# Kernel optimization log

Measured on AMD Instinct MI355X. Metric: run time of the kernel, lower is better.

Reference implementation:

```python
import jax, jax.numpy as jnp
import numpy as np
from jax import lax

TAU = 30.0  # softmax temperature


def setup_inputs() -> dict:
    key = jax.random.key(0)
    ks = jax.random.split(key, 6)
    N, Ci, Co, H, K, KW = 16, 64, 64, 256, 3, 4
    x = jax.random.normal(ks[0], (N, Ci, H, H), jnp.float32)
    # bank of KW candidate kernels: (Co, KW, Ci, K, K), kaiming-ish scale
    w_bank = jax.random.normal(ks[1], (Co, KW, Ci, K, K), jnp.float32) * (2.0 / (Co * K * K)) ** 0.5
    b_bank = jax.random.normal(ks[2], (Co, KW), jnp.float32) * 0.01
    # attention MLP (two 1x1 convs): Ci -> Ci//KW -> KW
    att_w1 = jax.random.normal(ks[3], (Ci // KW, Ci), jnp.float32) * (1.0 / Ci) ** 0.5
    att_b1 = jnp.zeros((Ci // KW,), jnp.float32)
    att_w2 = jax.random.normal(ks[4], (KW, Ci // KW), jnp.float32) * (KW / Ci) ** 0.5
    att_b2 = jnp.zeros((KW,), jnp.float32)
    return {"x": x, "w_bank": w_bank, "b_bank": b_bank,
            "att_w1": att_w1, "att_b1": att_b1, "att_w2": att_w2, "att_b2": att_b2}


def reference(x, w_bank, b_bank, att_w1, att_b1, att_w2, att_b2):
    # attention over weight banks: 1x1 conv -> ReLU -> 1x1 conv -> global avg pool -> softmax(/tau)
    h = jax.nn.relu(jnp.einsum('nchw,dc->ndhw', x, att_w1) + att_b1[None, :, None, None])
    logits = jnp.einsum('ndhw,ed->nehw', h, att_w2) + att_b2[None, :, None, None]
    pooled = jnp.mean(logits, axis=(2, 3))          # [N, KW] (avg_pool2d with kernel=H on square input)
    pi = jax.nn.softmax(pooled / TAU, axis=1)       # [N, KW]
    # per-sample aggregated kernels/biases
    w = jnp.einsum('okcij,nk->nocij', w_bank, pi)   # [N, Co, Ci, K, K]
    b = jnp.einsum('ok,nk->no', b_bank, pi)         # [N, Co]
    # per-sample conv (equivalent to the groups=N conv2d trick)
    def conv_one(xi, wi):
        return lax.conv_general_dilated(xi[None], wi, window_strides=(1, 1),
                                        padding=[(1, 1), (1, 1)],
                                        dimension_numbers=('NCHW', 'OIHW', 'NCHW'))[0]
    y = jax.vmap(conv_one)(x, w)                    # [N, Co, H, W]
    return y + b[:, :, None, None]
```

## Files before the change

kernel.cpp:

```cpp
#include <hip/hip_runtime.h>
#include <hip/hip_bf16.h>

typedef short short8 __attribute__((ext_vector_type(8)));
typedef float f32x4 __attribute__((ext_vector_type(4)));
typedef unsigned short ushort_t;

#define AS1 __attribute__((address_space(1)))
#define AS3 __attribute__((address_space(3)))

__device__ __forceinline__ ushort_t f2bf(float f) {
    unsigned u = __builtin_bit_cast(unsigned, f);
    unsigned r = (u + 0x7FFFu + ((u >> 16) & 1u)) >> 16;
    return (ushort_t)r;
}

__device__ __forceinline__ void gload_lds16(const void* g, void* l) {
    __builtin_amdgcn_global_load_lds((const AS1 unsigned*)g, (AS3 unsigned*)l, 16, 0, 0);
}

__global__ __launch_bounds__(256) void dc_k0_zeroborder(ushort_t* __restrict__ x_t)
{
    const int b = blockIdx.x, t = threadIdx.x;
    const int n = b >> 1, row = (b & 1) ? 257 : 0;
    short8 z = {0, 0, 0, 0, 0, 0, 0, 0};
    short8* p = reinterpret_cast<short8*>(x_t + (size_t)(n * 258 + row) * 258 * 64);
    for (int i = t; i < 2064; i += 256) p[i] = z;
}

__global__ __launch_bounds__(256) void dc_k1_stage_attn(
    const float* __restrict__ x, const float* __restrict__ w1,
    const float* __restrict__ b1, float* __restrict__ s_glob,
    ushort_t* __restrict__ x_t)
{
    __shared__ unsigned xt32[256 * 32];
    __shared__ ushort_t w1s[16 * 64];
    __shared__ float sacc[16];

    const int n = blockIdx.y, h = blockIdx.x, t = threadIdx.x;
    if (t < 16) sacc[t] = 0.f;
#pragma unroll
    for (int q = 0; q < 4; ++q) { int idx = q * 256 + t; w1s[idx] = f2bf(w1[idx]); }

    const float* xr = x + ((size_t)n * 64) * 65536 + (size_t)h * 256;
    const int sw = (t & 7) << 2;
    for (int cp = 0; cp < 32; ++cp) {
        float a = xr[(size_t)(2 * cp) * 65536 + t];
        float b = xr[(size_t)(2 * cp + 1) * 65536 + t];
        xt32[(t * 32 + cp) ^ sw] = (unsigned)f2bf(a) | ((unsigned)f2bf(b) << 16);
    }
    __syncthreads();

    const int lane = t & 63, wv = t >> 6, l15 = lane & 15, lg = lane >> 4;
    const short8* xt8 = reinterpret_cast<const short8*>(xt32);
    const short8* w18 = reinterpret_cast<const short8*>(w1s);

    short8 a0 = w18[l15 * 8 + lg];
    short8 a1 = w18[l15 * 8 + 4 + lg];
    float b1v[4];
#pragma unroll
    for (int r = 0; r < 4; ++r) b1v[r] = b1[lg * 4 + r];

    float rs[4] = {0.f, 0.f, 0.f, 0.f};
#pragma unroll
    for (int q = 0; q < 4; ++q) {
        int px = (wv * 4 + q) * 16 + l15;
        int pb = px * 8, ps = px & 7;
        short8 bb0 = xt8[pb + (lg ^ ps)];
        short8 bb1 = xt8[pb + ((4 + lg) ^ ps)];
        f32x4 hacc = {0.f, 0.f, 0.f, 0.f};
        hacc = __builtin_amdgcn_mfma_f32_16x16x32_bf16(a0, bb0, hacc, 0, 0, 0);
        hacc = __builtin_amdgcn_mfma_f32_16x16x32_bf16(a1, bb1, hacc, 0, 0, 0);
#pragma unroll
        for (int r = 0; r < 4; ++r) rs[r] += fmaxf(hacc[r] + b1v[r], 0.f);
    }
#pragma unroll
    for (int off = 1; off < 16; off <<= 1)
#pragma unroll
        for (int r = 0; r < 4; ++r) rs[r] += __shfl_xor(rs[r], off);
    if (l15 == 0) {
#pragma unroll
        for (int r = 0; r < 4; ++r) atomicAdd(&sacc[lg * 4 + r], rs[r]);
    }
    __syncthreads();
    if (t < 16) atomicAdd(&s_glob[n * 16 + t], sacc[t]);

    ushort_t* xo = x_t + (((size_t)n * 258 + h + 1) * 258 + 1) * 64;
    const int cb = t & 7, pxr = t >> 3;
#pragma unroll
    for (int rr = 0; rr < 8; ++rr) {
        int px = rr * 32 + pxr;
        short8 v = xt8[px * 8 + (cb ^ (px & 7))];
        *reinterpret_cast<short8*>(xo + (size_t)px * 64 + cb * 8) = v;
    }
    if (t < 16) {
        short8 z = {0, 0, 0, 0, 0, 0, 0, 0};
        size_t colbase = (((size_t)n * 258 + h + 1) * 258 + ((t < 8) ? 0 : 257)) * 64;
        reinterpret_cast<short8*>(x_t + colbase)[t & 7] = z;
    }
}

__global__ void dc_k2a_softmax_bias(
    const float* __restrict__ s_glob, const float* __restrict__ w2,
    const float* __restrict__ b2, const float* __restrict__ b_bank,
    float* __restrict__ pi, float* __restrict__ b_agg)
{
    __shared__ float piL[16][4];
    const int t = threadIdx.x;
    if (t < 16) {
        int n = t;
        float z[4];
#pragma unroll
        for (int e = 0; e < 4; ++e) {
            float p = 0.f;
            for (int d = 0; d < 16; ++d) p += w2[e * 16 + d] * s_glob[n * 16 + d];
            z[e] = (b2[e] + p * (1.f / 65536.f)) * (1.f / 30.f);
        }
        float m = fmaxf(fmaxf(z[0], z[1]), fmaxf(z[2], z[3]));
        float ex[4], sum = 0.f;
#pragma unroll
        for (int e = 0; e < 4; ++e) { ex[e] = expf(z[e] - m); sum += ex[e]; }
        float inv = 1.f / sum;
#pragma unroll
        for (int e = 0; e < 4; ++e) { float v = ex[e] * inv; pi[n * 4 + e] = v; piL[n][e] = v; }
    }
    __syncthreads();
    for (int r = 0; r < 16; ++r) {
        float v = 0.f;
#pragma unroll
        for (int kw = 0; kw < 4; ++kw) v += piL[r][kw] * b_bank[t * 4 + kw];
        b_agg[r * 64 + t] = v;
    }
}

__global__ void dc_k2b_aggw(const float* __restrict__ w_bank,
                            const float* __restrict__ pi,
                            ushort_t* __restrict__ A_frag)
{
    __shared__ float lw[2304];
    const int o = blockIdx.x, n = blockIdx.y, t = threadIdx.x;
    const float* wrow = w_bank + (size_t)o * 2304;
    for (int rr = 0; rr < 36; ++rr) lw[rr * 64 + t] = wrow[rr * 64 + t];
    float p0 = pi[n * 4 + 0], p1 = pi[n * 4 + 1], p2 = pi[n * 4 + 2], p3 = pi[n * 4 + 3];
    __syncthreads();
    const int c = t;
    const int cc = c >> 5, lg = (c >> 3) & 3, e = c & 7;
    const int mf = o >> 4, l15 = o & 15;
    ushort_t* base = A_frag + (size_t)n * 18 * 4 * 64 * 8;
#pragma unroll
    for (int ij = 0; ij < 9; ++ij) {
        float v = p0 * lw[0 * 576 + c * 9 + ij] + p1 * lw[1 * 576 + c * 9 + ij]
                + p2 * lw[2 * 576 + c * 9 + ij] + p3 * lw[3 * 576 + c * 9 + ij];
        int ks = ij * 2 + cc;
        base[(((ks * 4 + mf) * 64) + (lg * 16 + l15)) * 8 + e] = f2bf(v);
    }
}

__global__ __launch_bounds__(512, 1) void dc_k3_conv(
    const ushort_t* __restrict__ x_t, const ushort_t* __restrict__ A_frag,
    const float* __restrict__ b_agg, float* __restrict__ out)
{
    __shared__ char lds[73728 + 5 * 17408];
    char* ldsA = lds;
    char* ldsW = lds + 73728;

    int bid = blockIdx.x;
    int nb = (bid & 7) * 32 + (bid >> 3);
    const int n = nb >> 4;
    const int half = nb & 1;
    const int strip = (nb >> 1) & 7;
    const int h0 = strip * 32;
    const int w0 = half << 7;

    const int t = threadIdx.x, lane = t & 63, wv = t >> 6;
    const int l15 = lane & 15, lg = lane >> 4;
    const int pxl = wv * 16;

    const char* srcb = (const char*)x_t;
    const char* Asrc = (const char*)A_frag + (size_t)n * 73728;

    auto stage_row = [&](int rr, int slot) {
        size_t rowoff = ((size_t)(n * 258 + h0 + rr) * 258 + w0) * 128;
        char* dst = ldsW + slot * 17408;
        for (int k = wv; k < 17; k += 8) {
            unsigned q = k * 1024 + lane * 16;
            unsigned so = q ^ (((q >> 7) & 7) << 4);
            gload_lds16(srcb + rowoff + so, dst + k * 1024);
        }
    };

    for (int q = 0; q < 9; ++q) {
        int j = wv * 9 + q;
        gload_lds16(Asrc + j * 1024 + lane * 16, ldsA + j * 1024);
    }
    for (int r = 0; r < 4; ++r) stage_row(r, r);
    asm volatile("s_waitcnt vmcnt(0)" ::: "memory");
    __builtin_amdgcn_s_barrier();
    __builtin_amdgcn_sched_barrier(0);

    int boff[3][2];
#pragma unroll
    for (int kj = 0; kj < 3; ++kj)
#pragma unroll
        for (int cc = 0; cc < 2; ++cc) {
            int colL = pxl + l15 + kj;
            boff[kj][cc] = (colL * 128 + cc * 64 + lg * 16)
                           ^ ((colL & 7) << 4);
        }
    const int aoff = lane * 16;

    const float* bn = b_agg + n * 64;
    float bv[4][4];
#pragma unroll
    for (int mf = 0; mf < 4; ++mf)
#pragma unroll
        for (int r = 0; r < 4; ++r) bv[mf][r] = bn[mf * 16 + lg * 4 + r];

#pragma unroll 1
    for (int j = 0; j < 16; ++j) {
        const int r0 = 2 * j;
        const int r4 = r0 + 4, r5 = r0 + 5;

        if (r4 <= 33) stage_row(r4, r4 % 5);
        __builtin_amdgcn_sched_barrier(0);

        const char* sb[4] = { ldsW + (r0 % 5) * 17408,
                              ldsW + ((r0 + 1) % 5) * 17408,
                              ldsW + ((r0 + 2) % 5) * 17408,
                              ldsW + ((r0 + 3) % 5) * 17408 };

        f32x4 acc[4][2] = {};
        short8 afb[2][4], bfb[2][2];

#pragma unroll
        for (int mf = 0; mf < 4; ++mf)
            afb[0][mf] = *reinterpret_cast<const short8*>(ldsA + mf * 1024 + aoff);
#pragma unroll
        for (int o = 0; o < 2; ++o)
            bfb[0][o] = *reinterpret_cast<const short8*>(sb[o] + boff[0][0]);

#pragma unroll
        for (int ks = 0; ks < 18; ++ks) {
            if (ks == 6) {
                __builtin_amdgcn_s_barrier();
                if (r5 <= 33) stage_row(r5, r0 % 5);
                __builtin_amdgcn_sched_barrier(0);
            }
            const int cur = ks & 1, nxt = cur ^ 1;
            if (ks < 17) {
                const int k1 = ks + 1;
                const int ki1 = k1 / 6, rem = k1 % 6;
                const int kj1 = rem >> 1, cc1 = rem & 1;
#pragma unroll
                for (int mf = 0; mf < 4; ++mf)
                    afb[nxt][mf] = *reinterpret_cast<const short8*>(
                        ldsA + (k1 * 4 + mf) * 1024 + aoff);
#pragma unroll
                for (int o = 0; o < 2; ++o)
                    bfb[nxt][o] = *reinterpret_cast<const short8*>(
                        sb[ki1 + o] + boff[kj1][cc1]);
            }
            __builtin_amdgcn_s_setprio(1);
#pragma unroll
            for (int mf = 0; mf < 4; ++mf)
#pragma unroll
                for (int o = 0; o < 2; ++o)
                    acc[mf][o] = __builtin_amdgcn_mfma_f32_16x16x32_bf16(
                        afb[cur][mf], bfb[cur][o], acc[mf][o], 0, 0, 0);
            __builtin_amdgcn_s_setprio(0);
        }

#pragma unroll
        for (int o = 0; o < 2; ++o) {
            const int h = h0 + r0 + o;
#pragma unroll
            for (int mf = 0; mf < 4; ++mf) {
                const int col = w0 + pxl + l15;
#pragma unroll
                for (int r = 0; r < 4; ++r)
                    out[((size_t)(n * 64 + mf * 16 + lg * 4 + r) << 16)
                        + (size_t)h * 256 + col] = acc[mf][o][r] + bv[mf][r];
            }
        }
        __builtin_amdgcn_sched_barrier(0);
        asm volatile("s_waitcnt vmcnt(31)" ::: "memory");
        __builtin_amdgcn_s_barrier();
        __builtin_amdgcn_sched_barrier(0);
    }
}

extern "C" void kernel_launch(void* const* d_in, const int* in_sizes, int n_in,
                              void* d_out, int out_size, void* d_ws, size_t ws_size,
                              hipStream_t stream) {
    const float* x      = (const float*)d_in[0];
    const float* w_bank = (const float*)d_in[1];
    const float* b_bank = (const float*)d_in[2];
    const float* att_w1 = (const float*)d_in[3];
    const float* att_b1 = (const float*)d_in[4];
    const float* att_w2 = (const float*)d_in[5];
    const float* att_b2 = (const float*)d_in[6];
    float* out = (float*)d_out;

    char* ws = (char*)d_ws;
    float*    s_glob = (float*)ws;
    float*    pi     = (float*)(ws + 1024);
    float*    b_agg  = (float*)(ws + 2048);
    ushort_t* A_frag = (ushort_t*)(ws + 8192);
    ushort_t* x_t    = (ushort_t*)(ws + (2ull << 20));

    hipMemsetAsync(s_glob, 0, 16 * 16 * sizeof(float), stream);

    dc_k0_zeroborder<<<32, 256, 0, stream>>>(x_t);
    dc_k1_stage_attn<<<dim3(256, 16), 256, 0, stream>>>(x, att_w1, att_b1, s_glob, x_t);
    dc_k2a_softmax_bias<<<1, 64, 0, stream>>>(s_glob, att_w2, att_b2, b_bank, pi, b_agg);
    dc_k2b_aggw<<<dim3(64, 16), 64, 0, stream>>>(w_bank, pi, A_frag);
    dc_k3_conv<<<256, 512, 0, stream>>>(x_t, A_frag, b_agg, out);
}
```

Measured before the change: 190.9 us.

## Fuse small kernels, keep middle-row weights in registers, deepen conv row ring

Result: no change. 191.9 us (+0.5%).

```diff
diff --git a/kernel.cpp b/kernel.cpp
--- a/kernel.cpp
+++ b/kernel.cpp
@@ -16,15 +16,6 @@
 
 __device__ __forceinline__ void gload_lds16(const void* g, void* l) {
     __builtin_amdgcn_global_load_lds((const AS1 unsigned*)g, (AS3 unsigned*)l, 16, 0, 0);
-}
-
-__global__ __launch_bounds__(256) void dc_k0_zeroborder(ushort_t* __restrict__ x_t)
-{
-    const int b = blockIdx.x, t = threadIdx.x;
-    const int n = b >> 1, row = (b & 1) ? 257 : 0;
-    short8 z = {0, 0, 0, 0, 0, 0, 0, 0};
-    short8* p = reinterpret_cast<short8*>(x_t + (size_t)(n * 258 + row) * 258 * 64);
-    for (int i = t; i < 2064; i += 256) p[i] = z;
 }
 
 __global__ __launch_bounds__(256) void dc_k1_stage_attn(
@@ -37,6 +28,14 @@
     __shared__ float sacc[16];
 
     const int n = blockIdx.y, h = blockIdx.x, t = threadIdx.x;
+
+    if (h == 0 || h == 255) {
+        const int row = (h == 0) ? 0 : 257;
+        short8 z = {0, 0, 0, 0, 0, 0, 0, 0};
+        short8* p = reinterpret_cast<short8*>(x_t + (size_t)(n * 258 + row) * 258 * 64);
+        for (int i = t; i < 2064; i += 256) p[i] = z;
+    }
+
     if (t < 16) sacc[t] = 0.f;
 #pragma unroll
     for (int q = 0; q < 4; ++q) { int idx = q * 256 + t; w1s[idx] = f2bf(w1[idx]); }
@@ -99,49 +98,35 @@
     }
 }
 
-__global__ void dc_k2a_softmax_bias(
-    const float* __restrict__ s_glob, const float* __restrict__ w2,
-    const float* __restrict__ b2, const float* __restrict__ b_bank,
-    float* __restrict__ pi, float* __restrict__ b_agg)
-{
-    __shared__ float piL[16][4];
-    const int t = threadIdx.x;
-    if (t < 16) {
-        int n = t;
-        float z[4];
-#pragma unroll
-        for (int e = 0; e < 4; ++e) {
-            float p = 0.f;
-            for (int d = 0; d < 16; ++d) p += w2[e * 16 + d] * s_glob[n * 16 + d];
-            z[e] = (b2[e] + p * (1.f / 65536.f)) * (1.f / 30.f);
-        }
-        float m = fmaxf(fmaxf(z[0], z[1]), fmaxf(z[2], z[3]));
-        float ex[4], sum = 0.f;
-#pragma unroll
-        for (int e = 0; e < 4; ++e) { ex[e] = expf(z[e] - m); sum += ex[e]; }
-        float inv = 1.f / sum;
-#pragma unroll
-        for (int e = 0; e < 4; ++e) { float v = ex[e] * inv; pi[n * 4 + e] = v; piL[n][e] = v; }
-    }
-    __syncthreads();
-    for (int r = 0; r < 16; ++r) {
-        float v = 0.f;
-#pragma unroll
-        for (int kw = 0; kw < 4; ++kw) v += piL[r][kw] * b_bank[t * 4 + kw];
-        b_agg[r * 64 + t] = v;
-    }
-}
-
-__global__ void dc_k2b_aggw(const float* __restrict__ w_bank,
-                            const float* __restrict__ pi,
-                            ushort_t* __restrict__ A_frag)
+__global__ void dc_k2_agg(const float* __restrict__ s_glob,
+                          const float* __restrict__ w2,
+                          const float* __restrict__ b2,
+                          const float* __restrict__ b_bank,
+                          const float* __restrict__ w_bank,
+                          float* __restrict__ b_agg,
+                          ushort_t* __restrict__ A_frag)
 {
     __shared__ float lw[2304];
     const int o = blockIdx.x, n = blockIdx.y, t = threadIdx.x;
+
+    float z[4];
+#pragma unroll
+    for (int e = 0; e < 4; ++e) {
+        float p = 0.f;
+        for (int d = 0; d < 16; ++d) p += w2[e * 16 + d] * s_glob[n * 16 + d];
+        z[e] = (b2[e] + p * (1.f / 65536.f)) * (1.f / 30.f);
+    }
+    float m = fmaxf(fmaxf(z[0], z[1]), fmaxf(z[2], z[3]));
+    float ex[4], sum = 0.f;
+#pragma unroll
+    for (int e = 0; e < 4; ++e) { ex[e] = expf(z[e] - m); sum += ex[e]; }
+    float inv = 1.f / sum;
+    const float p0 = ex[0] * inv, p1 = ex[1] * inv, p2 = ex[2] * inv, p3 = ex[3] * inv;
+
     const float* wrow = w_bank + (size_t)o * 2304;
     for (int rr = 0; rr < 36; ++rr) lw[rr * 64 + t] = wrow[rr * 64 + t];
-    float p0 = pi[n * 4 + 0], p1 = pi[n * 4 + 1], p2 = pi[n * 4 + 2], p3 = pi[n * 4 + 3];
     __syncthreads();
+
     const int c = t;
     const int cc = c >> 5, lg = (c >> 3) & 3, e = c & 7;
     const int mf = o >> 4, l15 = o & 15;
@@ -153,15 +138,18 @@
         int ks = ij * 2 + cc;
         base[(((ks * 4 + mf) * 64) + (lg * 16 + l15)) * 8 + e] = f2bf(v);
     }
+    if (t == 0)
+        b_agg[n * 64 + o] = p0 * b_bank[o * 4 + 0] + p1 * b_bank[o * 4 + 1]
+                          + p2 * b_bank[o * 4 + 2] + p3 * b_bank[o * 4 + 3];
 }
 
 __global__ __launch_bounds__(512, 1) void dc_k3_conv(
     const ushort_t* __restrict__ x_t, const ushort_t* __restrict__ A_frag,
     const float* __restrict__ b_agg, float* __restrict__ out)
 {
-    __shared__ char lds[73728 + 5 * 17408];
+    __shared__ char lds[49152 + 6 * 17408];
     char* ldsA = lds;
-    char* ldsW = lds + 73728;
+    char* ldsW = lds + 49152;
 
     int bid = blockIdx.x;
     int nb = (bid & 7) * 32 + (bid >> 3);
@@ -188,11 +176,19 @@
         }
     };
 
-    for (int q = 0; q < 9; ++q) {
-        int j = wv * 9 + q;
-        gload_lds16(Asrc + j * 1024 + lane * 16, ldsA + j * 1024);
-    }
-    for (int r = 0; r < 4; ++r) stage_row(r, r);
+    for (int q = 0; q < 6; ++q) {
+        int jc = wv * 6 + q;
+        int gj = (jc < 24) ? jc : jc + 24;
+        gload_lds16(Asrc + gj * 1024 + lane * 16, ldsA + jc * 1024);
+    }
+    short8 aki1[6][4];
+#pragma unroll
+    for (int s = 0; s < 6; ++s)
+#pragma unroll
+        for (int mf = 0; mf < 4; ++mf)
+            aki1[s][mf] = *reinterpret_cast<const short8*>(
+                Asrc + ((6 + s) * 4 + mf) * 1024 + lane * 16);
+    for (int r = 0; r < 6; ++r) stage_row(r, r);
     asm volatile("s_waitcnt vmcnt(0)" ::: "memory");
     __builtin_amdgcn_s_barrier();
     __builtin_amdgcn_sched_barrier(0);
@@ -218,15 +214,12 @@
 #pragma unroll 1
     for (int j = 0; j < 16; ++j) {
         const int r0 = 2 * j;
-        const int r4 = r0 + 4, r5 = r0 + 5;
-
-        if (r4 <= 33) stage_row(r4, r4 % 5);
-        __builtin_amdgcn_sched_barrier(0);
-
-        const char* sb[4] = { ldsW + (r0 % 5) * 17408,
-                              ldsW + ((r0 + 1) % 5) * 17408,
-                              ldsW + ((r0 + 2) % 5) * 17408,
-                              ldsW + ((r0 + 3) % 5) * 17408 };
+        const int r6 = r0 + 6, r7 = r0 + 7;
+
+        const char* sb[4] = { ldsW + (r0 % 6) * 17408,
+                              ldsW + ((r0 + 1) % 6) * 17408,
+                              ldsW + ((r0 + 2) % 6) * 17408,
+                              ldsW + ((r0 + 3) % 6) * 17408 };
 
         f32x4 acc[4][2] = {};
         short8 afb[2][4], bfb[2][2];
@@ -237,27 +230,79 @@
 #pragma unroll
         for (int o = 0; o < 2; ++o)
             bfb[0][o] = *reinterpret_cast<const short8*>(sb[o] + boff[0][0]);
-
-#pragma unroll
-        for (int ks = 0; ks < 18; ++ks) {
-            if (ks == 6) {
-                __builtin_amdgcn_s_barrier();
-                if (r5 <= 33) stage_row(r5, r0 % 5);
-                __builtin_amdgcn_sched_barrier(0);
-            }
-            const int cur = ks & 1, nxt = cur ^ 1;
-            if (ks < 17) {
-                const int k1 = ks + 1;
-                const int ki1 = k1 / 6, rem = k1 % 6;
-                const int kj1 = rem >> 1, cc1 = rem & 1;
+#pragma unroll
+        for (int s = 0; s < 6; ++s) {
+            const int cur = s & 1, nxt = cur ^ 1;
+            if (s < 5) {
+                const int k1 = s + 1;
 #pragma unroll
                 for (int mf = 0; mf < 4; ++mf)
                     afb[nxt][mf] = *reinterpret_cast<const short8*>(
-                        ldsA + (k1 * 4 + mf) * 1024 + aoff);
+                        ldsA + k1 * 4096 + mf * 1024 + aoff);
 #pragma unroll
                 for (int o = 0; o < 2; ++o)
                     bfb[nxt][o] = *reinterpret_cast<const short8*>(
-                        sb[ki1 + o] + boff[kj1][cc1]);
+                        sb[o] + boff[k1 >> 1][k1 & 1]);
+            }
+            __builtin_amdgcn_s_setprio(1);
+#pragma unroll
+            for (int mf = 0; mf < 4; ++mf)
+#pragma unroll
+                for (int o = 0; o < 2; ++o)
+                    acc[mf][o] = __builtin_amdgcn_mfma_f32_16x16x32_bf16(
+                        afb[cur][mf], bfb[cur][o], acc[mf][o], 0, 0, 0);
+            __builtin_amdgcn_s_setprio(0);
+        }
+        __builtin_amdgcn_s_barrier();
+        if (r6 <= 33) stage_row(r6, r0 % 6);
+        __builtin_amdgcn_sched_barrier(0);
+
+#pragma unroll
+        for (int o = 0; o < 2; ++o)
+            bfb[0][o] = *reinterpret_cast<const short8*>(sb[1 + o] + boff[0][0]);
+#pragma unroll
+        for (int s = 0; s < 6; ++s) {
+            const int cur = s & 1, nxt = cur ^ 1;
+            if (s < 5) {
+                const int k1 = s + 1;
+#pragma unroll
+                for (int o = 0; o < 2; ++o)
+                    bfb[nxt][o] = *reinterpret_cast<const short8*>(
+                        sb[1 + o] + boff[k1 >> 1][k1 & 1]);
+            }
+            __builtin_amdgcn_s_setprio(1);
+#pragma unroll
+            for (int mf = 0; mf < 4; ++mf)
+#pragma unroll
+                for (int o = 0; o < 2; ++o)
+                    acc[mf][o] = __builtin_amdgcn_mfma_f32_16x16x32_bf16(
+                        aki1[s][mf], bfb[cur][o], acc[mf][o], 0, 0, 0);
+            __builtin_amdgcn_s_setprio(0);
+        }
+        __builtin_amdgcn_s_barrier();
+        if (r7 <= 33) stage_row(r7, (r0 + 1) % 6);
+        __builtin_amdgcn_sched_barrier(0);
+
+#pragma unroll
+        for (int mf = 0; mf < 4; ++mf)
+            afb[0][mf] = *reinterpret_cast<const short8*>(
+                ldsA + 6 * 4096 + mf * 1024 + aoff);
+#pragma unroll
+        for (int o = 0; o < 2; ++o)
+            bfb[0][o] = *reinterpret_cast<const short8*>(sb[2 + o] + boff[0][0]);
+#pragma unroll
+        for (int s = 0; s < 6; ++s) {
+            const int cur = s & 1, nxt = cur ^ 1;
+            if (s < 5) {
+                const int k1 = s + 1;
+#pragma unroll
+                for (int mf = 0; mf < 4; ++mf)
+                    afb[nxt][mf] = *reinterpret_cast<const short8*>(
+                        ldsA + (6 + k1) * 4096 + mf * 1024 + aoff);
+#pragma unroll
+                for (int o = 0; o < 2; ++o)
+                    bfb[nxt][o] = *reinterpret_cast<const short8*>(
+                        sb[2 + o] + boff[k1 >> 1][k1 & 1]);
             }
             __builtin_amdgcn_s_setprio(1);
 #pragma unroll
@@ -282,7 +327,7 @@
             }
         }
         __builtin_amdgcn_sched_barrier(0);
-        asm volatile("s_waitcnt vmcnt(31)" ::: "memory");
+        asm volatile("s_waitcnt vmcnt(38)" ::: "memory");
         __builtin_amdgcn_s_barrier();
         __builtin_amdgcn_sched_barrier(0);
     }
@@ -302,16 +347,14 @@
 
     char* ws = (char*)d_ws;
     float*    s_glob = (float*)ws;
-    float*    pi     = (float*)(ws + 1024);
     float*    b_agg  = (float*)(ws + 2048);
     ushort_t* A_frag = (ushort_t*)(ws + 8192);
     ushort_t* x_t    = (ushort_t*)(ws + (2ull << 20));
 
     hipMemsetAsync(s_glob, 0, 16 * 16 * sizeof(float), stream);
 
-    dc_k0_zeroborder<<<32, 256, 0, stream>>>(x_t);
     dc_k1_stage_attn<<<dim3(256, 16), 256, 0, stream>>>(x, att_w1, att_b1, s_glob, x_t);
-    dc_k2a_softmax_bias<<<1, 64, 0, stream>>>(s_glob, att_w2, att_b2, b_bank, pi, b_agg);
-    dc_k2b_aggw<<<dim3(64, 16), 64, 0, stream>>>(w_bank, pi, A_frag);
+    dc_k2_agg<<<dim3(64, 16), 64, 0, stream>>>(s_glob, att_w2, att_b2, b_bank,
+                                               w_bank, b_agg, A_frag);
     dc_k3_conv<<<256, 512, 0, stream>>>(x_t, A_frag, b_agg, out);
 }
```

## Fold small kernels into neighbours and preload B fragments per kernel row

Applied to the files above, without the earlier changes.

New measurement: 189.8 us (median of 2 runs). Within noise of the previous version (-0.6%).

```diff
diff --git a/kernel.cpp b/kernel.cpp
--- a/kernel.cpp
+++ b/kernel.cpp
@@ -16,15 +16,6 @@
 
 __device__ __forceinline__ void gload_lds16(const void* g, void* l) {
     __builtin_amdgcn_global_load_lds((const AS1 unsigned*)g, (AS3 unsigned*)l, 16, 0, 0);
-}
-
-__global__ __launch_bounds__(256) void dc_k0_zeroborder(ushort_t* __restrict__ x_t)
-{
-    const int b = blockIdx.x, t = threadIdx.x;
-    const int n = b >> 1, row = (b & 1) ? 257 : 0;
-    short8 z = {0, 0, 0, 0, 0, 0, 0, 0};
-    short8* p = reinterpret_cast<short8*>(x_t + (size_t)(n * 258 + row) * 258 * 64);
-    for (int i = t; i < 2064; i += 256) p[i] = z;
 }
 
 __global__ __launch_bounds__(256) void dc_k1_stage_attn(
@@ -37,6 +28,14 @@
     __shared__ float sacc[16];
 
     const int n = blockIdx.y, h = blockIdx.x, t = threadIdx.x;
+
+    if (h == 0 || h == 255) {
+        const int row = (h == 0) ? 0 : 257;
+        short8 z = {0, 0, 0, 0, 0, 0, 0, 0};
+        short8* p = reinterpret_cast<short8*>(x_t + (size_t)(n * 258 + row) * 258 * 64);
+        for (int i = t; i < 2064; i += 256) p[i] = z;
+    }
+
     if (t < 16) sacc[t] = 0.f;
 #pragma unroll
     for (int q = 0; q < 4; ++q) { int idx = q * 256 + t; w1s[idx] = f2bf(w1[idx]); }
@@ -99,49 +98,35 @@
     }
 }
 
-__global__ void dc_k2a_softmax_bias(
-    const float* __restrict__ s_glob, const float* __restrict__ w2,
-    const float* __restrict__ b2, const float* __restrict__ b_bank,
-    float* __restrict__ pi, float* __restrict__ b_agg)
-{
-    __shared__ float piL[16][4];
-    const int t = threadIdx.x;
-    if (t < 16) {
-        int n = t;
-        float z[4];
-#pragma unroll
-        for (int e = 0; e < 4; ++e) {
-            float p = 0.f;
-            for (int d = 0; d < 16; ++d) p += w2[e * 16 + d] * s_glob[n * 16 + d];
-            z[e] = (b2[e] + p * (1.f / 65536.f)) * (1.f / 30.f);
-        }
-        float m = fmaxf(fmaxf(z[0], z[1]), fmaxf(z[2], z[3]));
-        float ex[4], sum = 0.f;
-#pragma unroll
-        for (int e = 0; e < 4; ++e) { ex[e] = expf(z[e] - m); sum += ex[e]; }
-        float inv = 1.f / sum;
-#pragma unroll
-        for (int e = 0; e < 4; ++e) { float v = ex[e] * inv; pi[n * 4 + e] = v; piL[n][e] = v; }
-    }
-    __syncthreads();
-    for (int r = 0; r < 16; ++r) {
-        float v = 0.f;
-#pragma unroll
-        for (int kw = 0; kw < 4; ++kw) v += piL[r][kw] * b_bank[t * 4 + kw];
-        b_agg[r * 64 + t] = v;
-    }
-}
-
-__global__ void dc_k2b_aggw(const float* __restrict__ w_bank,
-                            const float* __restrict__ pi,
-                            ushort_t* __restrict__ A_frag)
+__global__ void dc_k2_agg(const float* __restrict__ s_glob,
+                          const float* __restrict__ w2,
+                          const float* __restrict__ b2,
+                          const float* __restrict__ b_bank,
+                          const float* __restrict__ w_bank,
+                          float* __restrict__ b_agg,
+                          ushort_t* __restrict__ A_frag)
 {
     __shared__ float lw[2304];
     const int o = blockIdx.x, n = blockIdx.y, t = threadIdx.x;
+
+    float z[4];
+#pragma unroll
+    for (int e = 0; e < 4; ++e) {
+        float p = 0.f;
+        for (int d = 0; d < 16; ++d) p += w2[e * 16 + d] * s_glob[n * 16 + d];
+        z[e] = (b2[e] + p * (1.f / 65536.f)) * (1.f / 30.f);
+    }
+    float m = fmaxf(fmaxf(z[0], z[1]), fmaxf(z[2], z[3]));
+    float ex[4], sum = 0.f;
+#pragma unroll
+    for (int e = 0; e < 4; ++e) { ex[e] = expf(z[e] - m); sum += ex[e]; }
+    float inv = 1.f / sum;
+    const float p0 = ex[0] * inv, p1 = ex[1] * inv, p2 = ex[2] * inv, p3 = ex[3] * inv;
+
     const float* wrow = w_bank + (size_t)o * 2304;
     for (int rr = 0; rr < 36; ++rr) lw[rr * 64 + t] = wrow[rr * 64 + t];
-    float p0 = pi[n * 4 + 0], p1 = pi[n * 4 + 1], p2 = pi[n * 4 + 2], p3 = pi[n * 4 + 3];
     __syncthreads();
+
     const int c = t;
     const int cc = c >> 5, lg = (c >> 3) & 3, e = c & 7;
     const int mf = o >> 4, l15 = o & 15;
@@ -153,6 +138,9 @@
         int ks = ij * 2 + cc;
         base[(((ks * 4 + mf) * 64) + (lg * 16 + l15)) * 8 + e] = f2bf(v);
     }
+    if (t == 0)
+        b_agg[n * 64 + o] = p0 * b_bank[o * 4 + 0] + p1 * b_bank[o * 4 + 1]
+                          + p2 * b_bank[o * 4 + 2] + p3 * b_bank[o * 4 + 3];
 }
 
 __global__ __launch_bounds__(512, 1) void dc_k3_conv(
@@ -229,44 +217,47 @@
                               ldsW + ((r0 + 3) % 5) * 17408 };
 
         f32x4 acc[4][2] = {};
-        short8 afb[2][4], bfb[2][2];
-
-#pragma unroll
-        for (int mf = 0; mf < 4; ++mf)
-            afb[0][mf] = *reinterpret_cast<const short8*>(ldsA + mf * 1024 + aoff);
-#pragma unroll
-        for (int o = 0; o < 2; ++o)
-            bfb[0][o] = *reinterpret_cast<const short8*>(sb[o] + boff[0][0]);
-
-#pragma unroll
-        for (int ks = 0; ks < 18; ++ks) {
-            if (ks == 6) {
+
+#pragma unroll
+        for (int ki = 0; ki < 3; ++ki) {
+            short8 bph[6][2];
+#pragma unroll
+            for (int s = 0; s < 6; ++s)
+#pragma unroll
+                for (int o = 0; o < 2; ++o)
+                    bph[s][o] = *reinterpret_cast<const short8*>(
+                        sb[ki + o] + boff[s >> 1][s & 1]);
+
+            short8 afb[2][4];
+#pragma unroll
+            for (int mf = 0; mf < 4; ++mf)
+                afb[0][mf] = *reinterpret_cast<const short8*>(
+                    ldsA + (ki * 6) * 4096 + mf * 1024 + aoff);
+
+#pragma unroll
+            for (int s = 0; s < 6; ++s) {
+                const int cur = s & 1, nxt = cur ^ 1;
+                if (s < 5) {
+#pragma unroll
+                    for (int mf = 0; mf < 4; ++mf)
+                        afb[nxt][mf] = *reinterpret_cast<const short8*>(
+                            ldsA + (ki * 6 + s + 1) * 4096 + mf * 1024 + aoff);
+                }
+                __builtin_amdgcn_s_setprio(1);
+#pragma unroll
+                for (int mf = 0; mf < 4; ++mf)
+#pragma unroll
+                    for (int o = 0; o < 2; ++o)
+                        acc[mf][o] = __builtin_amdgcn_mfma_f32_16x16x32_bf16(
+                            afb[cur][mf], bph[s][o], acc[mf][o], 0, 0, 0);
+                __builtin_amdgcn_s_setprio(0);
+            }
+
+            if (ki == 0) {
                 __builtin_amdgcn_s_barrier();
                 if (r5 <= 33) stage_row(r5, r0 % 5);
                 __builtin_amdgcn_sched_barrier(0);
             }
-            const int cur = ks & 1, nxt = cur ^ 1;
-            if (ks < 17) {
-                const int k1 = ks + 1;
-                const int ki1 = k1 / 6, rem = k1 % 6;
-                const int kj1 = rem >> 1, cc1 = rem & 1;
-#pragma unroll
-                for (int mf = 0; mf < 4; ++mf)
-                    afb[nxt][mf] = *reinterpret_cast<const short8*>(
-                        ldsA + (k1 * 4 + mf) * 1024 + aoff);
-#pragma unroll
-                for (int o = 0; o < 2; ++o)
-                    bfb[nxt][o] = *reinterpret_cast<const short8*>(
-                        sb[ki1 + o] + boff[kj1][cc1]);
-            }
-            __builtin_amdgcn_s_setprio(1);
-#pragma unroll
-            for (int mf = 0; mf < 4; ++mf)
-#pragma unroll
-                for (int o = 0; o < 2; ++o)
-                    acc[mf][o] = __builtin_amdgcn_mfma_f32_16x16x32_bf16(
-                        afb[cur][mf], bfb[cur][o], acc[mf][o], 0, 0, 0);
-            __builtin_amdgcn_s_setprio(0);
         }
 
 #pragma unroll
@@ -302,16 +293,14 @@
 
     char* ws = (char*)d_ws;
     float*    s_glob = (float*)ws;
-    float*    pi     = (float*)(ws + 1024);
     float*    b_agg  = (float*)(ws + 2048);
     ushort_t* A_frag = (ushort_t*)(ws + 8192);
     ushort_t* x_t    = (ushort_t*)(ws + (2ull << 20));
 
     hipMemsetAsync(s_glob, 0, 16 * 16 * sizeof(float), stream);
 
-    dc_k0_zeroborder<<<32, 256, 0, stream>>>(x_t);
     dc_k1_stage_attn<<<dim3(256, 16), 256, 0, stream>>>(x, att_w1, att_b1, s_glob, x_t);
-    dc_k2a_softmax_bias<<<1, 64, 0, stream>>>(s_glob, att_w2, att_b2, b_bank, pi, b_agg);
-    dc_k2b_aggw<<<dim3(64, 16), 64, 0, stream>>>(w_bank, pi, A_frag);
+    dc_k2_agg<<<dim3(64, 16), 64, 0, stream>>>(s_glob, att_w2, att_b2, b_bank,
+                                               w_bank, b_agg, A_frag);
     dc_k3_conv<<<256, 512, 0, stream>>>(x_t, A_frag, b_agg, out);
 }
```
